# Performance work log

Measured on AMD Instinct MI355X. Metric: run time of the kernel, lower is better.

Reference implementation:

```python
import jax, jax.numpy as jnp
import numpy as np

B, T, D, H, OUT = 1024, 2048, 5, 64, 128


def _lstm_layer(x, Wih, Whh, bih, bhh):
    """PyTorch-convention LSTM layer. x: [B,T,Din]; gate order i,f,g,o."""
    b, t = x.shape[0], x.shape[1]
    h = Whh.shape[1]
    # Precompute input projections for all timesteps (the only big GEMM).
    xp = jnp.einsum('btd,gd->btg', x, Wih) + bih + bhh        # [B,T,4H]
    xp = jnp.swapaxes(xp, 0, 1)                               # [T,B,4H]

    def step(carry, xt):
        hprev, cprev = carry
        gates = xt + hprev @ Whh.T                            # [B,4H]
        i, f, g, o = jnp.split(gates, 4, axis=-1)
        i = jax.nn.sigmoid(i)
        f = jax.nn.sigmoid(f)
        g = jnp.tanh(g)
        o = jax.nn.sigmoid(o)
        c = f * cprev + i * g
        hnew = o * jnp.tanh(c)
        return (hnew, c), hnew

    h0 = jnp.zeros((b, h), x.dtype)
    (hT, cT), hs = jax.lax.scan(step, (h0, h0), xp)
    return jnp.swapaxes(hs, 0, 1), hT                         # [B,T,H], [B,H]


def setup_inputs() -> dict:
    key = jax.random.key(0)
    ks = jax.random.split(key, 11)
    s = 1.0 / np.sqrt(H)  # PyTorch LSTM init range

    def u(k, shape):
        return jax.random.uniform(k, shape, jnp.float32, -s, s)

    return {
        'x': jax.random.normal(ks[0], (B, T, D), jnp.float32),
        'W_ih0': u(ks[1], (4 * H, D)),
        'W_hh0': u(ks[2], (4 * H, H)),
        'b_ih0': u(ks[3], (4 * H,)),
        'b_hh0': u(ks[4], (4 * H,)),
        'W_ih1': u(ks[5], (4 * H, H)),
        'W_hh1': u(ks[6], (4 * H, H)),
        'b_ih1': u(ks[7], (4 * H,)),
        'b_hh1': u(ks[8], (4 * H,)),
        'W_fc': u(ks[9], (OUT, H)),
        'b_fc': u(ks[10], (OUT,)),
    }


def reference(x, W_ih0, W_hh0, b_ih0, b_hh0, W_ih1, W_hh1, b_ih1, b_hh1, W_fc, b_fc):
    # Layer 1 over raw 5-dim signal; inter-layer dropout is inactive at inference.
    y1, _ = _lstm_layer(x, W_ih0, W_hh0, b_ih0, b_hh0)
    # Layer 2; only its final hidden state hn[-1] is used downstream.
    _, h2 = _lstm_layer(y1, W_ih1, W_hh1, b_ih1, b_hh1)
    return jax.nn.relu(h2 @ W_fc.T + b_fc)                    # [B,128]
```

## Files before the change

kernel.cpp:

```cpp
#include <hip/hip_runtime.h>
#include <math.h>

#define BATCH 1024
#define TSEQ  2048
#define DIN   5
#define H     64
#define BT    4
#define SSTR  160
#define NOUT  128

typedef _Float16 f16x8 __attribute__((ext_vector_type(8)));
typedef float    f32x4 __attribute__((ext_vector_type(4)));

#if __has_builtin(__builtin_amdgcn_rcpf)
__device__ __forceinline__ float rcp_fast(float x) { return __builtin_amdgcn_rcpf(x); }
#else
__device__ __forceinline__ float rcp_fast(float x) { return 1.0f / x; }
#endif

#define LOG2E 1.44269504088896f

__device__ __forceinline__ float sigm2(float s) {
    return rcp_fast(1.0f + __builtin_amdgcn_exp2f(-s));
}
__device__ __forceinline__ float tanh2(float s) {
    return fmaf(-2.0f, rcp_fast(__builtin_amdgcn_exp2f(s) + 1.0f), 1.0f);
}

__global__ __launch_bounds__(512)
void lstm_mfma(const float* __restrict__ x,
               const float* __restrict__ Wih0, const float* __restrict__ Whh0,
               const float* __restrict__ bih0, const float* __restrict__ bhh0,
               const float* __restrict__ Wih1, const float* __restrict__ Whh1,
               const float* __restrict__ bih1, const float* __restrict__ bhh1,
               const float* __restrict__ Wfc,  const float* __restrict__ bfc,
               float* __restrict__ out)
{
    __shared__ alignas(16) _Float16 S[2][BT * SSTR];
    __shared__ alignas(16) float    h2f[BT][H];

    const int tid  = threadIdx.x;
    const int w    = tid >> 6;
    const int lane = tid & 63;
    const int col  = lane & 15;
    const int q    = lane >> 4;
    const int ww   = w & 3;
    const int lay  = w >> 2;
    const int hu   = 16 * ww + col;
    const int b0   = blockIdx.x * BT;

    for (int j = tid; j < 2 * BT * SSTR; j += 512)
        ((_Float16*)S)[j] = (_Float16)0.0f;

    const float sgl[4] = {LOG2E, LOG2E, 2.0f * LOG2E, LOG2E};

    f16x8 Bf[4][4];
    f32x4 bC[4];
    #pragma unroll
    for (int g = 0; g < 4; ++g) {
        const int   row = g * 64 + hu;
        const float sg  = sgl[g];
        const float* Wa = lay ? (Wih1 + row * H) : (Whh0 + row * H);
        f16x8 f0, f1, f2, f3;
        #pragma unroll
        for (int j = 0; j < 8; ++j) {
            f0[j] = (_Float16)(Wa[q * 8 + j] * sg);
            f1[j] = (_Float16)(Wa[32 + q * 8 + j] * sg);
        }
        if (lay) {
            const float* Wb = Whh1 + row * H;
            #pragma unroll
            for (int j = 0; j < 8; ++j) {
                f2[j] = (_Float16)(Wb[q * 8 + j] * sg);
                f3[j] = (_Float16)(Wb[32 + q * 8 + j] * sg);
            }
        } else {
            #pragma unroll
            for (int j = 0; j < 8; ++j) {
                const int kk = q * 8 + j;
                f2[j] = (_Float16)(kk < DIN ? Wih0[row * DIN + kk] * sg : 0.0f);
                f3[j] = (_Float16)0.0f;
            }
        }
        Bf[g][0] = f0; Bf[g][1] = f1; Bf[g][2] = f2; Bf[g][3] = f3;
        const float bb = (lay ? (bih1[row] + bhh1[row])
                              : (bih0[row] + bhh0[row])) * sg;
        bC[g] = f32x4{bb, bb, bb, bb};
    }

    const bool xlane = (lay == 0) && (lane < DIN);
    __syncthreads();
    if (xlane)
        S[1][ww * SSTR + 128 + lane] =
            (_Float16)x[(size_t)(b0 + ww) * TSEQ * DIN + lane];

    const int abase = (col >> 2) * SSTR + q * 8;
    const int aoff2 = lay ? 64 : 128;
    float cst = 0.0f, h2fin = 0.0f;

    __syncthreads();

    #pragma unroll 1
    for (int i = 0; i <= TSEQ; ++i) {
        const _Float16* rb = S[(i + 1) & 1];
        _Float16*       wb = S[i & 1];

        float xn = 0.0f;
        const bool xld = xlane && (i + 1 < TSEQ);
        if (xld)
            xn = x[(size_t)(b0 + ww) * TSEQ * DIN + (i + 1) * DIN + lane];

        f16x8 a0 = *(const f16x8*)&rb[abase];
        f16x8 a1 = *(const f16x8*)&rb[abase + 32];
        f16x8 a2 = *(const f16x8*)&rb[abase + aoff2];
        f16x8 a3 = *(const f16x8*)&rb[abase + 96];

        f32x4 d[4];
        #pragma unroll
        for (int g = 0; g < 4; ++g) {
            d[g] = __builtin_amdgcn_mfma_f32_16x16x32_f16(a0, Bf[g][0], bC[g], 0, 0, 0);
            d[g] = __builtin_amdgcn_mfma_f32_16x16x32_f16(a1, Bf[g][1], d[g], 0, 0, 0);
            d[g] = __builtin_amdgcn_mfma_f32_16x16x32_f16(a2, Bf[g][2], d[g], 0, 0, 0);
        }
        if (lay) {
            #pragma unroll
            for (int g = 0; g < 4; ++g)
                d[g] = __builtin_amdgcn_mfma_f32_16x16x32_f16(a3, Bf[g][3], d[g], 0, 0, 0);
        }

        const bool act = lay ? (i > 0) : (i < TSEQ);
        if (act) {
            float iv = sigm2(d[0][0]);
            float fv = sigm2(d[1][0]);
            float gv = tanh2(d[2][0]);
            float ov = sigm2(d[3][0]);
            cst = fmaf(fv, cst, iv * gv);
            float h = ov * tanh2(2.0f * LOG2E * cst);
            wb[q * SSTR + lay * 64 + hu] = (_Float16)h;
            h2fin = h;
        }
        if (xld)
            wb[ww * SSTR + 128 + lane] = (_Float16)xn;

        __syncthreads();
    }

    if (lay) h2f[q][hu] = h2fin;
    __syncthreads();
    {
        const int e = tid >> 7;
        const int o = tid & (NOUT - 1);
        const float4* wr = (const float4*)(Wfc + o * H);
        const float*  hv = h2f[e];
        float s0 = 0.f, s1 = 0.f, s2 = 0.f, s3 = 0.f;
        #pragma unroll
        for (int k = 0; k < H / 4; ++k) {
            float4 wv = wr[k];
            s0 = fmaf(wv.x, hv[4 * k + 0], s0);
            s1 = fmaf(wv.y, hv[4 * k + 1], s1);
            s2 = fmaf(wv.z, hv[4 * k + 2], s2);
            s3 = fmaf(wv.w, hv[4 * k + 3], s3);
        }
        float acc = bfc[o] + (s0 + s1) + (s2 + s3);
        out[(size_t)(b0 + e) * NOUT + o] = fmaxf(acc, 0.0f);
    }
}

extern "C" void kernel_launch(void* const* d_in, const int* in_sizes, int n_in,
                              void* d_out, int out_size, void* d_ws, size_t ws_size,
                              hipStream_t stream) {
    const float* x    = (const float*)d_in[0];
    const float* Wih0 = (const float*)d_in[1];
    const float* Whh0 = (const float*)d_in[2];
    const float* bih0 = (const float*)d_in[3];
    const float* bhh0 = (const float*)d_in[4];
    const float* Wih1 = (const float*)d_in[5];
    const float* Whh1 = (const float*)d_in[6];
    const float* bih1 = (const float*)d_in[7];
    const float* bhh1 = (const float*)d_in[8];
    const float* Wfc  = (const float*)d_in[9];
    const float* bfc  = (const float*)d_in[10];
    float* out = (float*)d_out;

    lstm_mfma<<<dim3(BATCH / BT), dim3(512), 0, stream>>>(
        x, Wih0, Whh0, bih0, bhh0, Wih1, Whh1, bih1, bhh1, Wfc, bfc, out);
}
```

Measured before the change: 1.050 ms.

## Merge both LSTM layers into each wave, halving block size to 256 threads

Previously each block ran 8 waves, with 4 waves on layer 1 and 4 on layer 2. Now each of 4 waves computes both layers' gates for its 16 hidden units, holding both sets of weight fragments in registers. This halves the threads that take part in each per-step barrier and lets two independent MFMA chains interleave within one wave. In exchange it doubles serial MFMA and activation work per wave, raises register pressure, and may lower latency hiding across waves. The final FC stage is reworked so each thread computes two batch rows.

```diff
diff --git a/kernel.cpp b/kernel.cpp
--- a/kernel.cpp
+++ b/kernel.cpp
@@ -27,7 +27,7 @@
     return fmaf(-2.0f, rcp_fast(__builtin_amdgcn_exp2f(s) + 1.0f), 1.0f);
 }
 
-__global__ __launch_bounds__(512)
+__global__ __launch_bounds__(256)
 void lstm_mfma(const float* __restrict__ x,
                const float* __restrict__ Wih0, const float* __restrict__ Whh0,
                const float* __restrict__ bih0, const float* __restrict__ bhh0,
@@ -44,59 +44,57 @@
     const int lane = tid & 63;
     const int col  = lane & 15;
     const int q    = lane >> 4;
-    const int ww   = w & 3;
-    const int lay  = w >> 2;
-    const int hu   = 16 * ww + col;
+    const int hu   = 16 * w + col;
     const int b0   = blockIdx.x * BT;
 
-    for (int j = tid; j < 2 * BT * SSTR; j += 512)
+    for (int j = tid; j < 2 * BT * SSTR; j += 256)
         ((_Float16*)S)[j] = (_Float16)0.0f;
 
     const float sgl[4] = {LOG2E, LOG2E, 2.0f * LOG2E, LOG2E};
 
-    f16x8 Bf[4][4];
-    f32x4 bC[4];
+    f16x8 B1[4][3];
+    f16x8 B2[4][4];
+    f32x4 bC1[4], bC2[4];
     #pragma unroll
     for (int g = 0; g < 4; ++g) {
         const int   row = g * 64 + hu;
         const float sg  = sgl[g];
-        const float* Wa = lay ? (Wih1 + row * H) : (Whh0 + row * H);
-        f16x8 f0, f1, f2, f3;
-        #pragma unroll
-        for (int j = 0; j < 8; ++j) {
-            f0[j] = (_Float16)(Wa[q * 8 + j] * sg);
-            f1[j] = (_Float16)(Wa[32 + q * 8 + j] * sg);
-        }
-        if (lay) {
-            const float* Wb = Whh1 + row * H;
+        #pragma unroll
+        for (int kt = 0; kt < 2; ++kt) {
+            f16x8 f0, f1, f2;
             #pragma unroll
             for (int j = 0; j < 8; ++j) {
-                f2[j] = (_Float16)(Wb[q * 8 + j] * sg);
-                f3[j] = (_Float16)(Wb[32 + q * 8 + j] * sg);
+                f0[j] = (_Float16)(Whh0[row * H + kt * 32 + q * 8 + j] * sg);
+                f1[j] = (_Float16)(Wih1[row * H + kt * 32 + q * 8 + j] * sg);
+                f2[j] = (_Float16)(Whh1[row * H + kt * 32 + q * 8 + j] * sg);
             }
-        } else {
+            B1[g][kt]     = f0;
+            B2[g][kt]     = f1;
+            B2[g][2 + kt] = f2;
+        }
+        {
+            f16x8 f;
             #pragma unroll
             for (int j = 0; j < 8; ++j) {
                 const int kk = q * 8 + j;
-                f2[j] = (_Float16)(kk < DIN ? Wih0[row * DIN + kk] * sg : 0.0f);
-                f3[j] = (_Float16)0.0f;
+                f[j] = (_Float16)(kk < DIN ? Wih0[row * DIN + kk] * sg : 0.0f);
             }
-        }
-        Bf[g][0] = f0; Bf[g][1] = f1; Bf[g][2] = f2; Bf[g][3] = f3;
-        const float bb = (lay ? (bih1[row] + bhh1[row])
-                              : (bih0[row] + bhh0[row])) * sg;
-        bC[g] = f32x4{bb, bb, bb, bb};
+            B1[g][2] = f;
+        }
+        const float b1 = (bih0[row] + bhh0[row]) * sg;
+        const float b2 = (bih1[row] + bhh1[row]) * sg;
+        bC1[g] = f32x4{b1, b1, b1, b1};
+        bC2[g] = f32x4{b2, b2, b2, b2};
     }
 
-    const bool xlane = (lay == 0) && (lane < DIN);
+    const bool xlane = (lane < DIN);
     __syncthreads();
     if (xlane)
-        S[1][ww * SSTR + 128 + lane] =
-            (_Float16)x[(size_t)(b0 + ww) * TSEQ * DIN + lane];
+        S[1][w * SSTR + 128 + lane] =
+            (_Float16)x[(size_t)(b0 + w) * TSEQ * DIN + lane];
 
     const int abase = (col >> 2) * SSTR + q * 8;
-    const int aoff2 = lay ? 64 : 128;
-    float cst = 0.0f, h2fin = 0.0f;
+    float c1 = 0.0f, c2 = 0.0f, h2fin = 0.0f;
 
     __syncthreads();
 
@@ -108,61 +106,78 @@
         float xn = 0.0f;
         const bool xld = xlane && (i + 1 < TSEQ);
         if (xld)
-            xn = x[(size_t)(b0 + ww) * TSEQ * DIN + (i + 1) * DIN + lane];
+            xn = x[(size_t)(b0 + w) * TSEQ * DIN + (i + 1) * DIN + lane];
 
         f16x8 a0 = *(const f16x8*)&rb[abase];
         f16x8 a1 = *(const f16x8*)&rb[abase + 32];
-        f16x8 a2 = *(const f16x8*)&rb[abase + aoff2];
-        f16x8 a3 = *(const f16x8*)&rb[abase + 96];
-
-        f32x4 d[4];
+        f16x8 ah0 = *(const f16x8*)&rb[abase + 64];
+        f16x8 ah1 = *(const f16x8*)&rb[abase + 96];
+        f16x8 ax  = *(const f16x8*)&rb[abase + 128];
+
+        f32x4 d1[4], d2[4];
         #pragma unroll
         for (int g = 0; g < 4; ++g) {
-            d[g] = __builtin_amdgcn_mfma_f32_16x16x32_f16(a0, Bf[g][0], bC[g], 0, 0, 0);
-            d[g] = __builtin_amdgcn_mfma_f32_16x16x32_f16(a1, Bf[g][1], d[g], 0, 0, 0);
-            d[g] = __builtin_amdgcn_mfma_f32_16x16x32_f16(a2, Bf[g][2], d[g], 0, 0, 0);
-        }
-        if (lay) {
-            #pragma unroll
-            for (int g = 0; g < 4; ++g)
-                d[g] = __builtin_amdgcn_mfma_f32_16x16x32_f16(a3, Bf[g][3], d[g], 0, 0, 0);
-        }
-
-        const bool act = lay ? (i > 0) : (i < TSEQ);
-        if (act) {
-            float iv = sigm2(d[0][0]);
-            float fv = sigm2(d[1][0]);
-            float gv = tanh2(d[2][0]);
-            float ov = sigm2(d[3][0]);
-            cst = fmaf(fv, cst, iv * gv);
-            float h = ov * tanh2(2.0f * LOG2E * cst);
-            wb[q * SSTR + lay * 64 + hu] = (_Float16)h;
-            h2fin = h;
+            d1[g] = __builtin_amdgcn_mfma_f32_16x16x32_f16(a0, B1[g][0], bC1[g], 0, 0, 0);
+            d1[g] = __builtin_amdgcn_mfma_f32_16x16x32_f16(a1, B1[g][1], d1[g], 0, 0, 0);
+            d1[g] = __builtin_amdgcn_mfma_f32_16x16x32_f16(ax, B1[g][2], d1[g], 0, 0, 0);
+        }
+        #pragma unroll
+        for (int g = 0; g < 4; ++g) {
+            d2[g] = __builtin_amdgcn_mfma_f32_16x16x32_f16(a0,  B2[g][0], bC2[g], 0, 0, 0);
+            d2[g] = __builtin_amdgcn_mfma_f32_16x16x32_f16(a1,  B2[g][1], d2[g], 0, 0, 0);
+            d2[g] = __builtin_amdgcn_mfma_f32_16x16x32_f16(ah0, B2[g][2], d2[g], 0, 0, 0);
+            d2[g] = __builtin_amdgcn_mfma_f32_16x16x32_f16(ah1, B2[g][3], d2[g], 0, 0, 0);
+        }
+
+        if (i < TSEQ) {
+            float iv = sigm2(d1[0][0]);
+            float fv = sigm2(d1[1][0]);
+            float gv = tanh2(d1[2][0]);
+            float ov = sigm2(d1[3][0]);
+            c1 = fmaf(fv, c1, iv * gv);
+            wb[q * SSTR + hu] = (_Float16)(ov * tanh2(2.0f * LOG2E * c1));
+        }
+        if (i > 0) {
+            float iv = sigm2(d2[0][0]);
+            float fv = sigm2(d2[1][0]);
+            float gv = tanh2(d2[2][0]);
+            float ov = sigm2(d2[3][0]);
+            c2 = fmaf(fv, c2, iv * gv);
+            h2fin = ov * tanh2(2.0f * LOG2E * c2);
+            wb[q * SSTR + 64 + hu] = (_Float16)h2fin;
         }
         if (xld)
-            wb[ww * SSTR + 128 + lane] = (_Float16)xn;
+            wb[w * SSTR + 128 + lane] = (_Float16)xn;
 
         __syncthreads();
     }
 
-    if (lay) h2f[q][hu] = h2fin;
+    h2f[q][hu] = h2fin;
     __syncthreads();
     {
-        const int e = tid >> 7;
-        const int o = tid & (NOUT - 1);
+        const int o  = tid & (NOUT - 1);
+        const int e0 = tid >> 7;
         const float4* wr = (const float4*)(Wfc + o * H);
-        const float*  hv = h2f[e];
-        float s0 = 0.f, s1 = 0.f, s2 = 0.f, s3 = 0.f;
-        #pragma unroll
-        for (int k = 0; k < H / 4; ++k) {
-            float4 wv = wr[k];
-            s0 = fmaf(wv.x, hv[4 * k + 0], s0);
-            s1 = fmaf(wv.y, hv[4 * k + 1], s1);
-            s2 = fmaf(wv.z, hv[4 * k + 2], s2);
-            s3 = fmaf(wv.w, hv[4 * k + 3], s3);
-        }
-        float acc = bfc[o] + (s0 + s1) + (s2 + s3);
-        out[(size_t)(b0 + e) * NOUT + o] = fmaxf(acc, 0.0f);
+        float4 wv[H / 4];
+        #pragma unroll
+        for (int k = 0; k < H / 4; ++k) wv[k] = wr[k];
+        const float bo = bfc[o];
+        #pragma unroll
+        for (int rep = 0; rep < 2; ++rep) {
+            const int e = e0 + 2 * rep;
+            const float* hv = h2f[e];
+            float s0 = 0.f, s1 = 0.f, s2 = 0.f, s3 = 0.f;
+            #pragma unroll
+            for (int k = 0; k < H / 4; ++k) {
+                float4 v = wv[k];
+                s0 = fmaf(v.x, hv[4 * k + 0], s0);
+                s1 = fmaf(v.y, hv[4 * k + 1], s1);
+                s2 = fmaf(v.z, hv[4 * k + 2], s2);
+                s3 = fmaf(v.w, hv[4 * k + 3], s3);
+            }
+            float acc = bo + (s0 + s1) + (s2 + s3);
+            out[(size_t)(b0 + e) * NOUT + o] = fmaxf(acc, 0.0f);
+        }
     }
 }
 
@@ -182,6 +197,6 @@
     const float* bfc  = (const float*)d_in[10];
     float* out = (float*)d_out;
 
-    lstm_mfma<<<dim3(BATCH / BT), dim3(512), 0, stream>>>(
+    lstm_mfma<<<dim3(BATCH / BT), dim3(256), 0, stream>>>(
         x, Wih0, Whh0, bih0, bhh0, Wih1, Whh1, bih1, bhh1, Wfc, bfc, out);
 }
```

New measurement: 1.291 ms. 23.0% more time.

## Decouple LSTM layers with LDS ring buffers and atomic counter spin-waits

Applied to the files above, without the earlier changes.

Replaces the per-timestep block-wide barrier between the two layer wave groups with separate shared-memory ring buffers (depth 8) and workgroup-scoped atomic counters. Layer 1 can run up to DEP steps ahead of layer 2, which waits only on its own previous step and layer 1's output. The goal is to remove lockstep __syncthreads coupling so the two recurrences overlap freely. In exchange it adds spin-polling with s_sleep, atomic increments and fences each step, and relies on correct intra-wave ordering for the counters.

```diff
diff --git a/kernel.cpp b/kernel.cpp
--- a/kernel.cpp
+++ b/kernel.cpp
@@ -6,8 +6,10 @@
 #define DIN   5
 #define H     64
 #define BT    4
-#define SSTR  160
 #define NOUT  128
+#define DEP   8
+#define R1E   96
+#define R2E   80
 
 typedef _Float16 f16x8 __attribute__((ext_vector_type(8)));
 typedef float    f32x4 __attribute__((ext_vector_type(4)));
@@ -27,8 +29,13 @@
     return fmaf(-2.0f, rcp_fast(__builtin_amdgcn_exp2f(s) + 1.0f), 1.0f);
 }
 
+__device__ __forceinline__ void spin_ge(int* p, int v) {
+    while (__hip_atomic_load(p, __ATOMIC_ACQUIRE, __HIP_MEMORY_SCOPE_WORKGROUP) < v)
+        __builtin_amdgcn_s_sleep(1);
+}
+
 __global__ __launch_bounds__(512)
-void lstm_mfma(const float* __restrict__ x,
+void lstm_pipe(const float* __restrict__ x,
                const float* __restrict__ Wih0, const float* __restrict__ Whh0,
                const float* __restrict__ bih0, const float* __restrict__ bhh0,
                const float* __restrict__ Wih1, const float* __restrict__ Whh1,
@@ -36,8 +43,10 @@
                const float* __restrict__ Wfc,  const float* __restrict__ bfc,
                float* __restrict__ out)
 {
-    __shared__ alignas(16) _Float16 S[2][BT * SSTR];
+    __shared__ alignas(16) _Float16 ring1[DEP][BT * R1E];
+    __shared__ alignas(16) _Float16 ring2[DEP][BT * R2E];
     __shared__ alignas(16) float    h2f[BT][H];
+    __shared__ int done1, done2;
 
     const int tid  = threadIdx.x;
     const int w    = tid >> 6;
@@ -49,8 +58,9 @@
     const int hu   = 16 * ww + col;
     const int b0   = blockIdx.x * BT;
 
-    for (int j = tid; j < 2 * BT * SSTR; j += 512)
-        ((_Float16*)S)[j] = (_Float16)0.0f;
+    for (int j = tid; j < DEP * BT * R1E; j += 512) ((_Float16*)ring1)[j] = (_Float16)0.0f;
+    for (int j = tid; j < DEP * BT * R2E; j += 512) ((_Float16*)ring2)[j] = (_Float16)0.0f;
+    if (tid == 0) { done1 = 0; done2 = 0; }
 
     const float sgl[4] = {LOG2E, LOG2E, 2.0f * LOG2E, LOG2E};
 
@@ -88,65 +98,83 @@
         bC[g] = f32x4{bb, bb, bb, bb};
     }
 
-    const bool xlane = (lay == 0) && (lane < DIN);
     __syncthreads();
-    if (xlane)
-        S[1][ww * SSTR + 128 + lane] =
+    if (lay == 0 && lane < DIN)
+        ring1[DEP - 1][ww * R1E + 64 + lane] =
             (_Float16)x[(size_t)(b0 + ww) * TSEQ * DIN + lane];
-
-    const int abase = (col >> 2) * SSTR + q * 8;
-    const int aoff2 = lay ? 64 : 128;
-    float cst = 0.0f, h2fin = 0.0f;
-
     __syncthreads();
 
-    #pragma unroll 1
-    for (int i = 0; i <= TSEQ; ++i) {
-        const _Float16* rb = S[(i + 1) & 1];
-        _Float16*       wb = S[i & 1];
-
-        float xn = 0.0f;
-        const bool xld = xlane && (i + 1 < TSEQ);
-        if (xld)
-            xn = x[(size_t)(b0 + ww) * TSEQ * DIN + (i + 1) * DIN + lane];
-
-        f16x8 a0 = *(const f16x8*)&rb[abase];
-        f16x8 a1 = *(const f16x8*)&rb[abase + 32];
-        f16x8 a2 = *(const f16x8*)&rb[abase + aoff2];
-        f16x8 a3 = *(const f16x8*)&rb[abase + 96];
-
-        f32x4 d[4];
-        #pragma unroll
-        for (int g = 0; g < 4; ++g) {
-            d[g] = __builtin_amdgcn_mfma_f32_16x16x32_f16(a0, Bf[g][0], bC[g], 0, 0, 0);
-            d[g] = __builtin_amdgcn_mfma_f32_16x16x32_f16(a1, Bf[g][1], d[g], 0, 0, 0);
-            d[g] = __builtin_amdgcn_mfma_f32_16x16x32_f16(a2, Bf[g][2], d[g], 0, 0, 0);
-        }
-        if (lay) {
-            #pragma unroll
-            for (int g = 0; g < 4; ++g)
-                d[g] = __builtin_amdgcn_mfma_f32_16x16x32_f16(a3, Bf[g][3], d[g], 0, 0, 0);
-        }
-
-        const bool act = lay ? (i > 0) : (i < TSEQ);
-        if (act) {
+    if (lay == 0) {
+        const float* xp = x + (size_t)(b0 + ww) * TSEQ * DIN;
+        const int ab = (col >> 2) * R1E + q * 8;
+        float c1 = 0.0f;
+        #pragma unroll 1
+        for (int t = 0; t < TSEQ; ++t) {
+            if (t >= DEP) spin_ge(&done2, 4 * (t - DEP + 1));
+            spin_ge(&done1, 4 * t);
+            float xn = 0.0f;
+            const bool xld = (lane < DIN) && (t + 1 < TSEQ);
+            if (xld) xn = xp[(t + 1) * DIN + lane];
+
+            const _Float16* rb = ring1[(t + DEP - 1) % DEP];
+            f16x8 a0 = *(const f16x8*)&rb[ab];
+            f16x8 a1 = *(const f16x8*)&rb[ab + 32];
+            f16x8 ax = *(const f16x8*)&rb[ab + 64];
+            f32x4 d[4];
+            #pragma unroll
+            for (int g = 0; g < 4; ++g) {
+                d[g] = __builtin_amdgcn_mfma_f32_16x16x32_f16(a0, Bf[g][0], bC[g], 0, 0, 0);
+                d[g] = __builtin_amdgcn_mfma_f32_16x16x32_f16(a1, Bf[g][1], d[g], 0, 0, 0);
+                d[g] = __builtin_amdgcn_mfma_f32_16x16x32_f16(ax, Bf[g][2], d[g], 0, 0, 0);
+            }
             float iv = sigm2(d[0][0]);
             float fv = sigm2(d[1][0]);
             float gv = tanh2(d[2][0]);
             float ov = sigm2(d[3][0]);
-            cst = fmaf(fv, cst, iv * gv);
-            float h = ov * tanh2(2.0f * LOG2E * cst);
-            wb[q * SSTR + lay * 64 + hu] = (_Float16)h;
-            h2fin = h;
-        }
-        if (xld)
-            wb[ww * SSTR + 128 + lane] = (_Float16)xn;
-
-        __syncthreads();
+            c1 = fmaf(fv, c1, iv * gv);
+            _Float16* wb = ring1[t % DEP];
+            wb[q * R1E + hu] = (_Float16)(ov * tanh2(2.0f * LOG2E * c1));
+            if (xld) wb[ww * R1E + 64 + lane] = (_Float16)xn;
+            __threadfence_block();
+            if (lane == 0) atomicAdd(&done1, 1);
+        }
+    } else {
+        const int ab1 = (col >> 2) * R1E + q * 8;
+        const int ab2 = (col >> 2) * R2E + q * 8;
+        float c2 = 0.0f, h2fin = 0.0f;
+        #pragma unroll 1
+        for (int t = 0; t < TSEQ; ++t) {
+            spin_ge(&done2, 4 * t);
+            spin_ge(&done1, 4 * (t + 1));
+            const _Float16* ry = ring1[t % DEP];
+            const _Float16* rh = ring2[(t + DEP - 1) % DEP];
+            f16x8 ay0 = *(const f16x8*)&ry[ab1];
+            f16x8 ay1 = *(const f16x8*)&ry[ab1 + 32];
+            f16x8 ah0 = *(const f16x8*)&rh[ab2];
+            f16x8 ah1 = *(const f16x8*)&rh[ab2 + 32];
+            f32x4 d[4];
+            #pragma unroll
+            for (int g = 0; g < 4; ++g) {
+                d[g] = __builtin_amdgcn_mfma_f32_16x16x32_f16(ah0, Bf[g][2], bC[g], 0, 0, 0);
+                d[g] = __builtin_amdgcn_mfma_f32_16x16x32_f16(ah1, Bf[g][3], d[g], 0, 0, 0);
+                d[g] = __builtin_amdgcn_mfma_f32_16x16x32_f16(ay0, Bf[g][0], d[g], 0, 0, 0);
+                d[g] = __builtin_amdgcn_mfma_f32_16x16x32_f16(ay1, Bf[g][1], d[g], 0, 0, 0);
+            }
+            float iv = sigm2(d[0][0]);
+            float fv = sigm2(d[1][0]);
+            float gv = tanh2(d[2][0]);
+            float ov = sigm2(d[3][0]);
+            c2 = fmaf(fv, c2, iv * gv);
+            h2fin = ov * tanh2(2.0f * LOG2E * c2);
+            ring2[t % DEP][q * R2E + hu] = (_Float16)h2fin;
+            __threadfence_block();
+            if (lane == 0) atomicAdd(&done2, 1);
+        }
+        h2f[q][hu] = h2fin;
     }
 
-    if (lay) h2f[q][hu] = h2fin;
     __syncthreads();
+
     {
         const int e = tid >> 7;
         const int o = tid & (NOUT - 1);
@@ -182,6 +210,6 @@
     const float* bfc  = (const float*)d_in[10];
     float* out = (float*)d_out;
 
-    lstm_mfma<<<dim3(BATCH / BT), dim3(512), 0, stream>>>(
+    lstm_pipe<<<dim3(BATCH / BT), dim3(512), 0, stream>>>(
         x, Wih0, Whh0, bih0, bhh0, Wih1, Whh1, bih1, bhh1, Wfc, bfc, out);
 }
```

New measurement: 1.178 ms. +12.3%, slower.

## Compute layer-0 input projection off the recurrent critical path via register MFMA

Applied to the files above, without the earlier changes.

Layer-0 waves no longer stage x through shared memory. Each lane loads its own x row into a register fragment and runs the input-projection MFMA for step t+1 after the current step's activations, so the result is ready as the accumulator seed for the next step. This takes one dependent MFMA off the layer-0 recurrent chain and removes the x store to shared memory, and the shared row stride shrinks to 144. In exchange, every q==0 lane in layer 0 now issues its own global x load each step (redundant across lanes), the loop splits into two divergent per-layer branches, and dx adds register pressure.

```diff
diff --git a/kernel.cpp b/kernel.cpp
--- a/kernel.cpp
+++ b/kernel.cpp
@@ -6,7 +6,7 @@
 #define DIN   5
 #define H     64
 #define BT    4
-#define SSTR  160
+#define SSTR  144
 #define NOUT  128
 
 typedef _Float16 f16x8 __attribute__((ext_vector_type(8)));
@@ -88,14 +88,25 @@
         bC[g] = f32x4{bb, bb, bb, bb};
     }
 
-    const bool xlane = (lay == 0) && (lane < DIN);
-    __syncthreads();
-    if (xlane)
-        S[1][ww * SSTR + 128 + lane] =
-            (_Float16)x[(size_t)(b0 + ww) * TSEQ * DIN + lane];
-
-    const int abase = (col >> 2) * SSTR + q * 8;
-    const int aoff2 = lay ? 64 : 128;
+    const float* xp = x + (size_t)(b0 + (col >> 2)) * TSEQ * DIN;
+    f16x8 ax = {(_Float16)0.0f, (_Float16)0.0f, (_Float16)0.0f, (_Float16)0.0f,
+                (_Float16)0.0f, (_Float16)0.0f, (_Float16)0.0f, (_Float16)0.0f};
+    f32x4 dx[4];
+    if (lay == 0) {
+        if (q == 0) {
+            ax[0] = (_Float16)xp[0]; ax[1] = (_Float16)xp[1];
+            ax[2] = (_Float16)xp[2]; ax[3] = (_Float16)xp[3];
+            ax[4] = (_Float16)xp[4];
+        }
+        #pragma unroll
+        for (int g = 0; g < 4; ++g)
+            dx[g] = __builtin_amdgcn_mfma_f32_16x16x32_f16(ax, Bf[g][2], bC[g], 0, 0, 0);
+        xp += DIN;
+    }
+
+    const int ab  = (col >> 2) * SSTR + q * 8;
+    const int wb1 = q * SSTR + hu;
+    const int wb2 = q * SSTR + 64 + hu;
     float cst = 0.0f, h2fin = 0.0f;
 
     __syncthreads();
@@ -103,45 +114,61 @@
     #pragma unroll 1
     for (int i = 0; i <= TSEQ; ++i) {
         const _Float16* rb = S[(i + 1) & 1];
-        _Float16*       wb = S[i & 1];
-
-        float xn = 0.0f;
-        const bool xld = xlane && (i + 1 < TSEQ);
-        if (xld)
-            xn = x[(size_t)(b0 + ww) * TSEQ * DIN + (i + 1) * DIN + lane];
-
-        f16x8 a0 = *(const f16x8*)&rb[abase];
-        f16x8 a1 = *(const f16x8*)&rb[abase + 32];
-        f16x8 a2 = *(const f16x8*)&rb[abase + aoff2];
-        f16x8 a3 = *(const f16x8*)&rb[abase + 96];
-
-        f32x4 d[4];
-        #pragma unroll
-        for (int g = 0; g < 4; ++g) {
-            d[g] = __builtin_amdgcn_mfma_f32_16x16x32_f16(a0, Bf[g][0], bC[g], 0, 0, 0);
-            d[g] = __builtin_amdgcn_mfma_f32_16x16x32_f16(a1, Bf[g][1], d[g], 0, 0, 0);
-            d[g] = __builtin_amdgcn_mfma_f32_16x16x32_f16(a2, Bf[g][2], d[g], 0, 0, 0);
-        }
-        if (lay) {
+        _Float16*       wbuf = S[i & 1];
+
+        if (lay == 0) {
+            const bool xld = (q == 0) && (i + 1 < TSEQ);
+            float x0, x1, x2, x3, x4;
+            if (xld) { x0 = xp[0]; x1 = xp[1]; x2 = xp[2]; x3 = xp[3]; x4 = xp[4]; }
+
+            f16x8 a0 = *(const f16x8*)&rb[ab];
+            f16x8 a1 = *(const f16x8*)&rb[ab + 32];
+            f32x4 d[4];
+            #pragma unroll
+            for (int g = 0; g < 4; ++g) {
+                d[g] = __builtin_amdgcn_mfma_f32_16x16x32_f16(a0, Bf[g][0], dx[g], 0, 0, 0);
+                d[g] = __builtin_amdgcn_mfma_f32_16x16x32_f16(a1, Bf[g][1], d[g], 0, 0, 0);
+            }
+            if (i < TSEQ) {
+                float iv = sigm2(d[0][0]);
+                float fv = sigm2(d[1][0]);
+                float gv = tanh2(d[2][0]);
+                float ov = sigm2(d[3][0]);
+                cst = fmaf(fv, cst, iv * gv);
+                wbuf[wb1] = (_Float16)(ov * tanh2(2.0f * LOG2E * cst));
+            }
+            if (xld) {
+                ax[0] = (_Float16)x0; ax[1] = (_Float16)x1;
+                ax[2] = (_Float16)x2; ax[3] = (_Float16)x3;
+                ax[4] = (_Float16)x4;
+            }
             #pragma unroll
             for (int g = 0; g < 4; ++g)
-                d[g] = __builtin_amdgcn_mfma_f32_16x16x32_f16(a3, Bf[g][3], d[g], 0, 0, 0);
-        }
-
-        const bool act = lay ? (i > 0) : (i < TSEQ);
-        if (act) {
-            float iv = sigm2(d[0][0]);
-            float fv = sigm2(d[1][0]);
-            float gv = tanh2(d[2][0]);
-            float ov = sigm2(d[3][0]);
-            cst = fmaf(fv, cst, iv * gv);
-            float h = ov * tanh2(2.0f * LOG2E * cst);
-            wb[q * SSTR + lay * 64 + hu] = (_Float16)h;
-            h2fin = h;
-        }
-        if (xld)
-            wb[ww * SSTR + 128 + lane] = (_Float16)xn;
-
+                dx[g] = __builtin_amdgcn_mfma_f32_16x16x32_f16(ax, Bf[g][2], bC[g], 0, 0, 0);
+            xp += DIN;
+        } else {
+            f16x8 ay0 = *(const f16x8*)&rb[ab];
+            f16x8 ay1 = *(const f16x8*)&rb[ab + 32];
+            f16x8 ah0 = *(const f16x8*)&rb[ab + 64];
+            f16x8 ah1 = *(const f16x8*)&rb[ab + 96];
+            f32x4 d[4];
+            #pragma unroll
+            for (int g = 0; g < 4; ++g) {
+                d[g] = __builtin_amdgcn_mfma_f32_16x16x32_f16(ay0, Bf[g][0], bC[g], 0, 0, 0);
+                d[g] = __builtin_amdgcn_mfma_f32_16x16x32_f16(ay1, Bf[g][1], d[g], 0, 0, 0);
+                d[g] = __builtin_amdgcn_mfma_f32_16x16x32_f16(ah0, Bf[g][2], d[g], 0, 0, 0);
+                d[g] = __builtin_amdgcn_mfma_f32_16x16x32_f16(ah1, Bf[g][3], d[g], 0, 0, 0);
+            }
+            if (i > 0) {
+                float iv = sigm2(d[0][0]);
+                float fv = sigm2(d[1][0]);
+                float gv = tanh2(d[2][0]);
+                float ov = sigm2(d[3][0]);
+                cst = fmaf(fv, cst, iv * gv);
+                h2fin = ov * tanh2(2.0f * LOG2E * cst);
+                wbuf[wb2] = (_Float16)h2fin;
+            }
+        }
         __syncthreads();
     }
 
```

Result: faster. 988.6 us (-5.8%).
